# Kernel optimization log

Measured on AMD Instinct MI355X. Metric: run time of the kernel, lower is better.

The kernel has to match this reference:

```python
import jax, jax.numpy as jnp
import numpy as np

WS = 4        # window_size
SS = 2        # shift_size
NH = 8        # num_heads
EPS = 1e-5    # LayerNorm eps (torch default)


def _rel_pos_index(ws):
    coords = np.stack(np.meshgrid(np.arange(ws), np.arange(ws), indexing='ij')).reshape(2, -1)
    rel = (coords[:, :, None] - coords[:, None, :]).transpose(1, 2, 0)
    rel[..., 0] += ws - 1
    rel[..., 1] += ws - 1
    rel[..., 0] *= 2 * ws - 1
    return rel.sum(-1)  # [N, N] ints

REL_IDX = _rel_pos_index(WS)


def _shift_mask(Hp, Wp, ws, ss):
    # standard Swin shifted-window region mask: 0 within region, -100 across regions
    img = np.zeros((Hp, Wp))
    cnt = 0
    for hs in (slice(0, -ws), slice(-ws, -ss), slice(-ss, None)):
        for wsl in (slice(0, -ws), slice(-ws, -ss), slice(-ss, None)):
            img[hs, wsl] = cnt
            cnt += 1
    mw = img.reshape(Hp // ws, ws, Wp // ws, ws).transpose(0, 2, 1, 3).reshape(-1, ws * ws)
    d = mw[:, None, :] - mw[:, :, None]
    return np.where(d != 0, -100.0, 0.0).astype(np.float32)  # [nW, N, N]


def _ln(x, g, b):
    m = jnp.mean(x, -1, keepdims=True)
    v = jnp.mean((x - m) ** 2, -1, keepdims=True)
    return (x - m) * jax.lax.rsqrt(v + EPS) * g + b


def setup_inputs() -> dict:
    key = jax.random.key(0)
    ks = jax.random.split(key, 8)
    D, F = 512, 1024
    rn = lambda k, s: (jax.random.normal(k, s, jnp.float32) * 0.02)
    return {
        'x': jax.random.normal(ks[0], (4, 64 * 128, D), jnp.float32),
        'g1': jnp.ones((D,), jnp.float32), 'beta1': jnp.zeros((D,), jnp.float32),
        'w_qkv': rn(ks[1], (3 * D, D)), 'b_qkv': jnp.zeros((3 * D,), jnp.float32),
        'rpb': rn(ks[2], ((2 * WS - 1) ** 2, NH)),
        'w_proj': rn(ks[3], (D, D)), 'b_proj': jnp.zeros((D,), jnp.float32),
        'g2': jnp.ones((D,), jnp.float32), 'beta2': jnp.zeros((D,), jnp.float32),
        'w1': rn(ks[4], (F, D)), 'b1': jnp.zeros((F,), jnp.float32),
        'w2': rn(ks[5], (D, F)), 'b2': jnp.zeros((D,), jnp.float32),
        'H': 64, 'W': 128,
    }


def reference(x, g1, beta1, w_qkv, b_qkv, rpb, w_proj, b_proj, g2, beta2, w1, b1, w2, b2, H, W):
    B, L, C = x.shape
    hd = C // NH
    scale = hd ** (-0.5)
    N = WS * WS
    Hp, Wp = H, W  # H, W chosen divisible by WS -> no padding branch
    nW = (Hp // WS) * (Wp // WS)

    shortcut = x
    h = _ln(x, g1, beta1).reshape(B, H, W, C)
    # cyclic shift
    h = jnp.roll(h, (-SS, -SS), axis=(1, 2))
    # window partition -> [B*nW, N, C]
    xw = h.reshape(B, Hp // WS, WS, Wp // WS, WS, C).transpose(0, 1, 3, 2, 4, 5).reshape(-1, N, C)

    qkv = (xw @ w_qkv.T + b_qkv).reshape(-1, N, 3, NH, hd).transpose(2, 0, 3, 1, 4)
    q, k, v = qkv[0] * scale, qkv[1], qkv[2]          # [B*nW, NH, N, hd]
    attn = jnp.einsum('whnd,whmd->whnm', q, k)        # [B*nW, NH, N, N]

    bias = rpb[REL_IDX.reshape(-1)].reshape(N, N, NH).transpose(2, 0, 1)  # [NH, N, N]
    attn = attn + bias[None]

    mask = jnp.asarray(_shift_mask(Hp, Wp, WS, SS))   # [nW, N, N]
    attn = attn.reshape(B, nW, NH, N, N) + mask[None, :, None]
    attn = jax.nn.softmax(attn.reshape(-1, NH, N, N), axis=-1)

    o = jnp.einsum('whnm,whmd->whnd', attn, v).transpose(0, 2, 1, 3).reshape(-1, N, C)
    o = o @ w_proj.T + b_proj
    # window reverse + reverse shift
    o = o.reshape(B, Hp // WS, Wp // WS, WS, WS, C).transpose(0, 1, 3, 2, 4, 5).reshape(B, Hp, Wp, C)
    o = jnp.roll(o, (SS, SS), axis=(1, 2)).reshape(B, H * W, C)

    x = shortcut + o
    h2 = _ln(x, g2, beta2)
    m = jax.nn.gelu(h2 @ w1.T + b1, approximate=False) @ w2.T + b2
    return x + m
```

## Files before the change

kernel.cpp:

```cpp
#include <hip/hip_runtime.h>
#include <hip/hip_bf16.h>
#include <math.h>

typedef __bf16 bf16_t;
typedef __bf16 bf16x8 __attribute__((ext_vector_type(8)));
typedef __bf16 bf16x4 __attribute__((ext_vector_type(4)));
typedef float f32x4 __attribute__((ext_vector_type(4)));


#define X1_OFF   0u
#define XW_OFF   67108864u
#define QKV_OFF  100663296u
#define WQ_OFF   201326592u
#define WP_OFF   202899456u
#define W1_OFF   203423744u
#define W2_OFF   204472320u
#define SV_OFF   205520896u
#define FLAG_OFF 205545472u

__device__ __forceinline__ int perm_row(int r) {
    int b   = r >> 13;
    int rem = r & 8191;
    int w   = rem >> 4;
    int n   = rem & 15;
    int wy  = w >> 5, wx = w & 31;
    int y   = wy * 4 + (n >> 2);
    int x   = wx * 4 + (n & 3);
    int ys  = (y + 2) & 63;
    int xs  = (x + 2) & 127;
    return (b << 13) + (ys << 7) + xs;
}

__device__ __forceinline__ void gld16(const void* g, void* l) {
    __builtin_amdgcn_global_load_lds(
        (const __attribute__((address_space(1))) unsigned int*)(unsigned long long)(uintptr_t)g,
        (__attribute__((address_space(3))) unsigned int*)(unsigned int)(uintptr_t)l,
        16, 0, 0);
}

#define SBAR __builtin_amdgcn_sched_barrier(0)
#define BARRIER do { SBAR; __builtin_amdgcn_s_barrier(); SBAR; } while (0)

__device__ __forceinline__ float fast_gelu(float x) {
    float y = 0.7978845608f * (x + 0.044715f * x * x * x);
    y = fminf(fmaxf(y, -15.f), 15.f);
    float u = __builtin_amdgcn_exp2f(y * 2.885390082f);
    float t = (u - 1.f) / (u + 1.f);
    return 0.5f * x * (1.f + t);
}

__global__ __launch_bounds__(256) void k_probe(const unsigned short* __restrict__ x,
                                               int n, int* __restrict__ flag) {
    __shared__ int cnt;
    if (threadIdx.x == 0) cnt = 0;
    __syncthreads();
    int c = 0;
    for (int i = threadIdx.x; i < n; i += 256) {
        int e = (x[i] >> 7) & 0xFF;
        if (e >= 0xC0) c++;
    }
    atomicAdd(&cnt, c);
    __syncthreads();
    if (threadIdx.x == 0) *flag = (cnt > 8) ? 1 : 0;
}

__global__ __launch_bounds__(256) void k_cvt_bf16(const void* __restrict__ src,
                                                  bf16_t* __restrict__ dst, int n,
                                                  const int* __restrict__ flag) {
    int i = blockIdx.x * 256 + threadIdx.x;
    if (i >= n) return;
    if (*flag) dst[i] = (bf16_t)((const float*)src)[i];
    else       dst[i] = ((const bf16_t*)src)[i];
}

__global__ __launch_bounds__(256) void k_cvt_small(
        const void* g1, const void* be1, const void* bq, const void* bp,
        const void* g2, const void* be2, const void* b1, const void* b2,
        const void* rpb, float* __restrict__ dst, const int* __restrict__ flag) {
    int i = blockIdx.x * 256 + threadIdx.x;
    const void* src; int off;
    if      (i < 512)  { src = g1;  off = i; }
    else if (i < 1024) { src = be1; off = i - 512; }
    else if (i < 2560) { src = bq;  off = i - 1024; }
    else if (i < 3072) { src = bp;  off = i - 2560; }
    else if (i < 3584) { src = g2;  off = i - 3072; }
    else if (i < 4096) { src = be2; off = i - 3584; }
    else if (i < 5120) { src = b1;  off = i - 4096; }
    else if (i < 5632) { src = b2;  off = i - 5120; }
    else if (i < 6024) { src = rpb; off = i - 5632; }
    else return;
    if (*flag) dst[i] = ((const float*)src)[off];
    else       dst[i] = (float)((const bf16_t*)src)[off];
}

__global__ __launch_bounds__(256) void k_ln1(const void* __restrict__ x,
                                             const float* __restrict__ g,
                                             const float* __restrict__ be,
                                             bf16_t* __restrict__ xw,
                                             const int* __restrict__ flag) {
    int r    = blockIdx.x * 4 + (threadIdx.x >> 6);
    int lane = threadIdx.x & 63;
    long ro  = (long)perm_row(r) * 512;
    int base = lane * 8;
    float v[8];
    if (*flag) {
        const float* p = (const float*)x + ro + base;
#pragma unroll
        for (int j = 0; j < 8; j++) v[j] = p[j];
    } else {
        bf16x8 p = *(const bf16x8*)((const bf16_t*)x + ro + base);
#pragma unroll
        for (int j = 0; j < 8; j++) v[j] = (float)p[j];
    }
    float s = 0.f, ss = 0.f;
#pragma unroll
    for (int j = 0; j < 8; j++) { s += v[j]; ss += v[j] * v[j]; }
#pragma unroll
    for (int off = 32; off; off >>= 1) {
        s  += __shfl_down(s,  off, 64);
        ss += __shfl_down(ss, off, 64);
    }
    s  = __shfl(s, 0, 64);
    ss = __shfl(ss, 0, 64);
    float m   = s * (1.f / 512.f);
    float var = ss * (1.f / 512.f) - m * m;
    float inv = rsqrtf(var + 1e-5f);
    bf16_t* orow = xw + (long)r * 512;
    bf16x8 o;
#pragma unroll
    for (int j = 0; j < 8; j++)
        o[j] = (bf16_t)((v[j] - m) * inv * g[base + j] + be[base + j]);
    *(bf16x8*)(orow + base) = o;
}

__global__ __launch_bounds__(256) void k_ln2(const float* __restrict__ x1,
                                             const float* __restrict__ g,
                                             const float* __restrict__ be,
                                             bf16_t* __restrict__ h2) {
    int r    = blockIdx.x * 4 + (threadIdx.x >> 6);
    int lane = threadIdx.x & 63;
    const float* xr = x1 + (long)r * 512;
    int base = lane * 8;
    float v[8];
    float s = 0.f, ss = 0.f;
#pragma unroll
    for (int j = 0; j < 8; j++) {
        float t = xr[base + j];
        v[j] = t; s += t; ss += t * t;
    }
#pragma unroll
    for (int off = 32; off; off >>= 1) {
        s  += __shfl_down(s,  off, 64);
        ss += __shfl_down(ss, off, 64);
    }
    s  = __shfl(s, 0, 64);
    ss = __shfl(ss, 0, 64);
    float m   = s * (1.f / 512.f);
    float var = ss * (1.f / 512.f) - m * m;
    float inv = rsqrtf(var + 1e-5f);
    bf16_t* orow = h2 + (long)r * 512;
    bf16x8 o;
#pragma unroll
    for (int j = 0; j < 8; j++)
        o[j] = (bf16_t)((v[j] - m) * inv * g[base + j] + be[base + j]);
    *(bf16x8*)(orow + base) = o;
}

template<int EPI>
__global__ __launch_bounds__(512, 2) void k_gemm256(const bf16_t* __restrict__ A,
                                                    const bf16_t* __restrict__ Wt,
                                                    const float* __restrict__ bias,
                                                    void* __restrict__ out,
                                                    const void* __restrict__ res,
                                                    const int* __restrict__ flag,
                                                    int N, int K) {
    __shared__ __attribute__((aligned(16))) char smem[131072];
    int tid  = threadIdx.x;
    int lane = tid & 63, wv = tid >> 6;

    int nbx = N >> 8;
    int id  = blockIdx.x;
    int xb  = (id >> 3) % nbx;
    int yb  = ((id >> 3) / nbx) * 8 + (id & 7);
    int m0  = yb << 8, n0 = xb << 8;

    int srow = tid >> 3;
    int cg   = (tid & 7) ^ (srow & 7);
    const bf16_t* gA = A  + (long)(m0 + srow) * K + cg * 8;
    const bf16_t* gB = Wt + (long)(n0 + srow) * K + cg * 8;
    long r64 = (long)64 * K;

    int rr = lane & 15, quad = lane >> 4;
    int wh = wv >> 2, wq = wv & 3;
    int lA  = (wh * 64 + rr) * 128;
    int lB  = (wq * 32 + rr) * 128;
    int ck0 = (quad ^ (rr & 7)) * 16;
    int ck1 = ck0 ^ 64;

    f32x4 acc[8][4];
#pragma unroll
    for (int mi = 0; mi < 8; mi++)
#pragma unroll
        for (int ni = 0; ni < 4; ni++) { f32x4 z = {0.f,0.f,0.f,0.f}; acc[mi][ni] = z; }

    int S = K >> 6;

    gld16(gA,             smem + 0     + wv * 1024);
    gld16(gA + r64,       smem + 8192  + wv * 1024);
    gld16(gB,             smem + 32768 + wv * 1024);
    gld16(gB + r64,       smem + 40960 + wv * 1024);
    gld16(gB + 2 * r64,   smem + 49152 + wv * 1024);
    gld16(gB + 3 * r64,   smem + 57344 + wv * 1024);
    gld16(gA + 2 * r64,   smem + 16384 + wv * 1024);
    gld16(gA + 3 * r64,   smem + 24576 + wv * 1024);
    asm volatile("s_waitcnt vmcnt(4)" ::: "memory");
    BARRIER;

    bf16x8 af[4][2], bg[2][2];

#define FRAG_A(AH)                                                            \
    _Pragma("unroll") for (int mi = 0; mi < 4; mi++) {                        \
        af[mi][0] = *(const bf16x8*)(bc + (AH)*16384 + lA + mi*2048 + ck0);   \
        af[mi][1] = *(const bf16x8*)(bc + (AH)*16384 + lA + mi*2048 + ck1);   \
    }
#define FRAG_B(BH)                                                            \
    _Pragma("unroll") for (int ni = 0; ni < 2; ni++) {                        \
        bg[ni][0] = *(const bf16x8*)(bc + 32768 + (BH)*16384 + lB + ni*2048 + ck0); \
        bg[ni][1] = *(const bf16x8*)(bc + 32768 + (BH)*16384 + lB + ni*2048 + ck1); \
    }
#define MFMA_CL(AH, BH)                                                       \
    do {                                                                      \
        asm volatile("s_waitcnt lgkmcnt(0)" ::: "memory"); SBAR;              \
        __builtin_amdgcn_s_setprio(1);                                        \
        _Pragma("unroll") for (int mi = 0; mi < 4; mi++)                      \
            _Pragma("unroll") for (int ni = 0; ni < 2; ni++)                  \
                _Pragma("unroll") for (int kk = 0; kk < 2; kk++)              \
                    acc[(AH)*4 + mi][(BH)*2 + ni] =                           \
                        __builtin_amdgcn_mfma_f32_16x16x32_bf16(              \
                            af[mi][kk], bg[ni][kk], acc[(AH)*4 + mi][(BH)*2 + ni], 0, 0, 0); \
        __builtin_amdgcn_s_setprio(0);                                        \
    } while (0)
#define STAGE(GP, SLOT)                                                       \
    do { gld16((GP) + kn,       bn + (SLOT) + wv * 1024);                     \
         gld16((GP) + r64 + kn, bn + (SLOT) + 8192 + wv * 1024); } while (0)

    for (int t = 0; t < S; ++t) {
        char* bc = smem + (t & 1) * 65536;
        char* bn = smem + ((t & 1) ^ 1) * 65536;
        long  kn = (long)(t + 1) * 64;
        bool  st = (t + 1 < S);
        FRAG_A(0); FRAG_B(0);
        if (st) { STAGE(gA, 0);
                  asm volatile("s_waitcnt vmcnt(4)" ::: "memory"); }
        else    { asm volatile("s_waitcnt vmcnt(2)" ::: "memory"); }
        BARRIER;
        MFMA_CL(0, 0);
        FRAG_B(1);
        if (st) { STAGE(gB, 32768);
                  asm volatile("s_waitcnt vmcnt(4)" ::: "memory"); }
        else    { asm volatile("s_waitcnt vmcnt(0)" ::: "memory"); }
        BARRIER;
        MFMA_CL(0, 1);
        FRAG_A(1);
        if (st) STAGE(gB + 2 * r64, 49152);
        BARRIER;
        MFMA_CL(1, 1);
        FRAG_B(0);
        if (st) { STAGE(gA + 2 * r64, 16384);
                  asm volatile("s_waitcnt vmcnt(4)" ::: "memory"); }
        BARRIER;
        MFMA_CL(1, 0);
    }
    BARRIER;
#undef FRAG_A
#undef FRAG_B
#undef MFMA_CL
#undef STAGE

    float* sc = (float*)(smem + wv * 16384);
    int f    = (EPI == 1 || EPI == 3) ? *flag : 0;
    int j8   = lane & 7;
    int rl   = lane >> 3;
    int colg = n0 + wq * 32 + (j8 >> 2) * 128 + ((j8 * 8) & 31);
    f32x4 b0 = *(const f32x4*)(bias + colg);
    f32x4 b1 = *(const f32x4*)(bias + colg + 4);

#pragma unroll
    for (int ah = 0; ah < 2; ++ah) {
#pragma unroll
        for (int bh = 0; bh < 2; ++bh)
#pragma unroll
            for (int ni = 0; ni < 2; ++ni)
#pragma unroll
                for (int mi = 0; mi < 4; ++mi)
#pragma unroll
                    for (int i = 0; i < 4; ++i) {
                        int r  = mi * 16 + quad * 4 + i;
                        int cl = bh * 32 + ni * 16 + rr;
                        sc[r * 64 + ((((cl >> 2) ^ (r & 15)) << 2) | (cl & 3))] =
                            acc[ah * 4 + mi][bh * 2 + ni][i];
                    }
#pragma unroll
        for (int p = 0; p < 8; ++p) {
            int r = p * 8 + rl;
            f32x4 v0 = *(const f32x4*)(sc + r * 64 + (((2 * j8)     ^ (r & 15)) << 2));
            f32x4 v1 = *(const f32x4*)(sc + r * 64 + (((2 * j8 + 1) ^ (r & 15)) << 2));
            int row = m0 + ah * 128 + wh * 64 + r;
            v0 += b0; v1 += b1;

            if (EPI == 0) {
                bf16x8 ob;
#pragma unroll
                for (int c = 0; c < 4; c++) { ob[c] = (bf16_t)v0[c]; ob[c + 4] = (bf16_t)v1[c]; }
                *(bf16x8*)((bf16_t*)out + (long)row * N + colg) = ob;
            } else if (EPI == 1) {
                long o = (long)perm_row(row) * 512 + colg;
                if (f) {
                    f32x4 r0 = *(const f32x4*)((const float*)res + o);
                    f32x4 r1 = *(const f32x4*)((const float*)res + o + 4);
                    v0 += r0; v1 += r1;
                } else {
                    bf16x8 rb = *(const bf16x8*)((const bf16_t*)res + o);
#pragma unroll
                    for (int c = 0; c < 4; c++) { v0[c] += (float)rb[c]; v1[c] += (float)rb[c + 4]; }
                }
                *(f32x4*)((float*)out + o)     = v0;
                *(f32x4*)((float*)out + o + 4) = v1;
            } else if (EPI == 2) {
                bf16x8 ob;
#pragma unroll
                for (int c = 0; c < 4; c++) {
                    ob[c]     = (bf16_t)fast_gelu(v0[c]);
                    ob[c + 4] = (bf16_t)fast_gelu(v1[c]);
                }
                *(bf16x8*)((bf16_t*)out + (long)row * N + colg) = ob;
            } else {
                long o = (long)row * 512 + colg;
                f32x4 r0 = *(const f32x4*)((const float*)res + o);
                f32x4 r1 = *(const f32x4*)((const float*)res + o + 4);
                v0 += r0; v1 += r1;
                if (f) {
                    *(f32x4*)((float*)out + o)     = v0;
                    *(f32x4*)((float*)out + o + 4) = v1;
                } else {
                    bf16x8 ob;
#pragma unroll
                    for (int c = 0; c < 4; c++) { ob[c] = (bf16_t)v0[c]; ob[c + 4] = (bf16_t)v1[c]; }
                    *(bf16x8*)((bf16_t*)out + o) = ob;
                }
            }
        }
    }
}

__global__ __launch_bounds__(256) void k_attn(const bf16_t* __restrict__ qkv,
                                              const float* __restrict__ rpb,
                                              bf16_t* __restrict__ O) {
    __shared__ float q[16][68], k[16][68], v[16][68];
    __shared__ float S[16][17];

    int blk = blockIdx.x;
    int h   = blk & 7;
    int w   = blk >> 3;
    int tid = threadIdx.x;

    int n0 = tid >> 4;
    int d0 = (tid & 15) * 4;
    const bf16_t* base = qkv + (long)(w * 16 + n0) * 1536 + h * 64 + d0;
    bf16x4 qv = *(const bf16x4*)(base);
    bf16x4 kv = *(const bf16x4*)(base + 512);
    bf16x4 vv = *(const bf16x4*)(base + 1024);
    f32x4 qf, kf, vf;
#pragma unroll
    for (int j = 0; j < 4; j++) {
        qf[j] = (float)qv[j] * 0.125f;
        kf[j] = (float)kv[j];
        vf[j] = (float)vv[j];
    }
    *(f32x4*)&q[n0][d0] = qf;
    *(f32x4*)&k[n0][d0] = kf;
    *(f32x4*)&v[n0][d0] = vf;
    __syncthreads();

    int i = tid >> 4, j = tid & 15;
    float s = 0.f;
#pragma unroll
    for (int d = 0; d < 64; d++) s += q[i][d] * k[j][d];

    int iy = i >> 2, ix = i & 3, jy = j >> 2, jx = j & 3;
    s += rpb[((iy - jy + 3) * 7 + (ix - jx + 3)) * 8 + h];

    int wl = w & 511;
    int wy = wl >> 5, wx = wl & 31;
    int yi = wy * 4 + iy, xi = wx * 4 + ix;
    int yj = wy * 4 + jy, xj = wx * 4 + jx;
    int ri = (yi < 60 ? 0 : (yi < 62 ? 1 : 2)) * 3 + (xi < 124 ? 0 : (xi < 126 ? 1 : 2));
    int rj = (yj < 60 ? 0 : (yj < 62 ? 1 : 2)) * 3 + (xj < 124 ? 0 : (xj < 126 ? 1 : 2));
    if (ri != rj) s -= 100.f;
    S[i][j] = s;
    __syncthreads();

    if (tid < 16) {
        float mx = -1e30f;
#pragma unroll
        for (int c = 0; c < 16; c++) mx = fmaxf(mx, S[tid][c]);
        float sum = 0.f;
#pragma unroll
        for (int c = 0; c < 16; c++) { float e = expf(S[tid][c] - mx); S[tid][c] = e; sum += e; }
        float invs = 1.f / sum;
#pragma unroll
        for (int c = 0; c < 16; c++) S[tid][c] *= invs;
    }
    __syncthreads();

#pragma unroll
    for (int t = 0; t < 4; t++) {
        int e  = tid + t * 256;
        int oi = e >> 6, od = e & 63;
        float acc = 0.f;
#pragma unroll
        for (int c = 0; c < 16; c++) acc += S[oi][c] * v[c][od];
        O[(long)(w * 16 + oi) * 512 + h * 64 + od] = (bf16_t)acc;
    }
}

extern "C" void kernel_launch(void* const* d_in, const int* in_sizes, int n_in,
                              void* d_out, int out_size, void* d_ws, size_t ws_size,
                              hipStream_t stream) {
    char* ws = (char*)d_ws;
    float*  x1   = (float*)(ws + X1_OFF);
    bf16_t* xw   = (bf16_t*)(ws + XW_OFF);
    bf16_t* qkv  = (bf16_t*)(ws + QKV_OFF);
    bf16_t* wq_b = (bf16_t*)(ws + WQ_OFF);
    bf16_t* wp_b = (bf16_t*)(ws + WP_OFF);
    bf16_t* w1_b = (bf16_t*)(ws + W1_OFF);
    bf16_t* w2_b = (bf16_t*)(ws + W2_OFF);
    float*  sv   = (float*)(ws + SV_OFF);
    int*    flag = (int*)(ws + FLAG_OFF);

    k_probe<<<1, 256, 0, stream>>>((const unsigned short*)d_in[0], 4096, flag);
    k_cvt_bf16<<<3072, 256, 0, stream>>>(d_in[3],  wq_b, 786432, flag);
    k_cvt_bf16<<<1024, 256, 0, stream>>>(d_in[6],  wp_b, 262144, flag);
    k_cvt_bf16<<<2048, 256, 0, stream>>>(d_in[10], w1_b, 524288, flag);
    k_cvt_bf16<<<2048, 256, 0, stream>>>(d_in[12], w2_b, 524288, flag);
    k_cvt_small<<<24,  256, 0, stream>>>(d_in[1], d_in[2], d_in[4], d_in[7],
                                         d_in[8], d_in[9], d_in[11], d_in[13],
                                         d_in[5], sv, flag);

    k_ln1<<<dim3(8192), dim3(256), 0, stream>>>(d_in[0], sv, sv + 512, xw, flag);
    k_gemm256<0><<<dim3(768), dim3(512), 0, stream>>>(xw, wq_b, sv + 1024, qkv, nullptr, flag, 1536, 512);
    k_attn<<<dim3(16384), dim3(256), 0, stream>>>(qkv, sv + 5632, xw );
    k_gemm256<1><<<dim3(256), dim3(512), 0, stream>>>(xw, wp_b, sv + 2560, x1, d_in[0], flag, 512, 512);
    k_ln2<<<dim3(8192), dim3(256), 0, stream>>>(x1, sv + 3072, sv + 3584, xw );
    k_gemm256<2><<<dim3(512), dim3(512), 0, stream>>>(xw, w1_b, sv + 4096, qkv , nullptr, flag, 1024, 512);
    k_gemm256<3><<<dim3(256), dim3(512), 0, stream>>>(qkv, w2_b, sv + 5120, d_out, x1, flag, 512, 1024);
}
```

Baseline: 427.8 us.

## Add 128x128 GEMM kernel for N=512 GEMMs and warp-shuffle attention softmax

Adds a smaller-tile 128x128 GEMM kernel (256 threads, 64KB LDS, double buffered) and uses it for the two N=512 GEMMs (proj and FC2). This raises the grid from 256 to 1024 blocks so the many CUs on the device are better occupied. The epilogue is factored into a shared helper. Separately, the attention softmax now uses 16-lane shuffle reductions across all threads instead of 16 serial threads, which removes one barrier.

```diff
diff --git a/kernel.cpp b/kernel.cpp
--- a/kernel.cpp
+++ b/kernel.cpp
@@ -164,6 +164,74 @@
     for (int j = 0; j < 8; j++)
         o[j] = (bf16_t)((v[j] - m) * inv * g[base + j] + be[base + j]);
     *(bf16x8*)(orow + base) = o;
+}
+
+template<int EPI>
+__device__ __forceinline__ void epi_block(float* sc, const f32x4* accp,
+                                          int quad, int rr, int rl, int j8,
+                                          int row0, int colg, f32x4 b0, f32x4 b1,
+                                          void* out, const void* res, int f, int N) {
+#pragma unroll
+    for (int ni = 0; ni < 4; ++ni)
+#pragma unroll
+        for (int mi = 0; mi < 4; ++mi)
+#pragma unroll
+            for (int i = 0; i < 4; ++i) {
+                int r  = mi * 16 + quad * 4 + i;
+                int cl = ni * 16 + rr;
+                sc[r * 64 + ((((cl >> 2) ^ (r & 15)) << 2) | (cl & 3))] =
+                    accp[mi * 4 + ni][i];
+            }
+#pragma unroll
+    for (int p = 0; p < 8; ++p) {
+        int r = p * 8 + rl;
+        f32x4 v0 = *(const f32x4*)(sc + r * 64 + (((2 * j8)     ^ (r & 15)) << 2));
+        f32x4 v1 = *(const f32x4*)(sc + r * 64 + (((2 * j8 + 1) ^ (r & 15)) << 2));
+        int row = row0 + r;
+        v0 += b0; v1 += b1;
+
+        if (EPI == 0) {
+            bf16x8 ob;
+#pragma unroll
+            for (int c = 0; c < 4; c++) { ob[c] = (bf16_t)v0[c]; ob[c + 4] = (bf16_t)v1[c]; }
+            *(bf16x8*)((bf16_t*)out + (long)row * N + colg) = ob;
+        } else if (EPI == 1) {
+            long o = (long)perm_row(row) * 512 + colg;
+            if (f) {
+                f32x4 r0 = *(const f32x4*)((const float*)res + o);
+                f32x4 r1 = *(const f32x4*)((const float*)res + o + 4);
+                v0 += r0; v1 += r1;
+            } else {
+                bf16x8 rb = *(const bf16x8*)((const bf16_t*)res + o);
+#pragma unroll
+                for (int c = 0; c < 4; c++) { v0[c] += (float)rb[c]; v1[c] += (float)rb[c + 4]; }
+            }
+            *(f32x4*)((float*)out + o)     = v0;
+            *(f32x4*)((float*)out + o + 4) = v1;
+        } else if (EPI == 2) {
+            bf16x8 ob;
+#pragma unroll
+            for (int c = 0; c < 4; c++) {
+                ob[c]     = (bf16_t)fast_gelu(v0[c]);
+                ob[c + 4] = (bf16_t)fast_gelu(v1[c]);
+            }
+            *(bf16x8*)((bf16_t*)out + (long)row * N + colg) = ob;
+        } else {
+            long o = (long)row * 512 + colg;
+            f32x4 r0 = *(const f32x4*)((const float*)res + o);
+            f32x4 r1 = *(const f32x4*)((const float*)res + o + 4);
+            v0 += r0; v1 += r1;
+            if (f) {
+                *(f32x4*)((float*)out + o)     = v0;
+                *(f32x4*)((float*)out + o + 4) = v1;
+            } else {
+                bf16x8 ob;
+#pragma unroll
+                for (int c = 0; c < 4; c++) { ob[c] = (bf16_t)v0[c]; ob[c + 4] = (bf16_t)v1[c]; }
+                *(bf16x8*)((bf16_t*)out + o) = ob;
+            }
+        }
+    }
 }
 
 template<int EPI>
@@ -287,77 +355,118 @@
 
 #pragma unroll
     for (int ah = 0; ah < 2; ++ah) {
+        f32x4 blk[16];
 #pragma unroll
         for (int bh = 0; bh < 2; ++bh)
 #pragma unroll
             for (int ni = 0; ni < 2; ++ni)
 #pragma unroll
                 for (int mi = 0; mi < 4; ++mi)
-#pragma unroll
-                    for (int i = 0; i < 4; ++i) {
-                        int r  = mi * 16 + quad * 4 + i;
-                        int cl = bh * 32 + ni * 16 + rr;
-                        sc[r * 64 + ((((cl >> 2) ^ (r & 15)) << 2) | (cl & 3))] =
-                            acc[ah * 4 + mi][bh * 2 + ni][i];
-                    }
-#pragma unroll
-        for (int p = 0; p < 8; ++p) {
-            int r = p * 8 + rl;
-            f32x4 v0 = *(const f32x4*)(sc + r * 64 + (((2 * j8)     ^ (r & 15)) << 2));
-            f32x4 v1 = *(const f32x4*)(sc + r * 64 + (((2 * j8 + 1) ^ (r & 15)) << 2));
-            int row = m0 + ah * 128 + wh * 64 + r;
-            v0 += b0; v1 += b1;
-
-            if (EPI == 0) {
-                bf16x8 ob;
-#pragma unroll
-                for (int c = 0; c < 4; c++) { ob[c] = (bf16_t)v0[c]; ob[c + 4] = (bf16_t)v1[c]; }
-                *(bf16x8*)((bf16_t*)out + (long)row * N + colg) = ob;
-            } else if (EPI == 1) {
-                long o = (long)perm_row(row) * 512 + colg;
-                if (f) {
-                    f32x4 r0 = *(const f32x4*)((const float*)res + o);
-                    f32x4 r1 = *(const f32x4*)((const float*)res + o + 4);
-                    v0 += r0; v1 += r1;
-                } else {
-                    bf16x8 rb = *(const bf16x8*)((const bf16_t*)res + o);
-#pragma unroll
-                    for (int c = 0; c < 4; c++) { v0[c] += (float)rb[c]; v1[c] += (float)rb[c + 4]; }
-                }
-                *(f32x4*)((float*)out + o)     = v0;
-                *(f32x4*)((float*)out + o + 4) = v1;
-            } else if (EPI == 2) {
-                bf16x8 ob;
-#pragma unroll
-                for (int c = 0; c < 4; c++) {
-                    ob[c]     = (bf16_t)fast_gelu(v0[c]);
-                    ob[c + 4] = (bf16_t)fast_gelu(v1[c]);
-                }
-                *(bf16x8*)((bf16_t*)out + (long)row * N + colg) = ob;
-            } else {
-                long o = (long)row * 512 + colg;
-                f32x4 r0 = *(const f32x4*)((const float*)res + o);
-                f32x4 r1 = *(const f32x4*)((const float*)res + o + 4);
-                v0 += r0; v1 += r1;
-                if (f) {
-                    *(f32x4*)((float*)out + o)     = v0;
-                    *(f32x4*)((float*)out + o + 4) = v1;
-                } else {
-                    bf16x8 ob;
-#pragma unroll
-                    for (int c = 0; c < 4; c++) { ob[c] = (bf16_t)v0[c]; ob[c + 4] = (bf16_t)v1[c]; }
-                    *(bf16x8*)((bf16_t*)out + o) = ob;
-                }
-            }
+                    blk[mi * 4 + (bh * 2 + ni)] = acc[ah * 4 + mi][bh * 2 + ni];
+        epi_block<EPI>(sc, blk, quad, rr, rl, j8,
+                       m0 + ah * 128 + wh * 64, colg, b0, b1, out, res, f, N);
+    }
+}
+
+template<int EPI>
+__global__ __launch_bounds__(256, 2) void k_gemm128(const bf16_t* __restrict__ A,
+                                                    const bf16_t* __restrict__ Wt,
+                                                    const float* __restrict__ bias,
+                                                    void* __restrict__ out,
+                                                    const void* __restrict__ res,
+                                                    const int* __restrict__ flag,
+                                                    int N, int K) {
+    __shared__ __attribute__((aligned(16))) char smem[65536];
+    int tid  = threadIdx.x;
+    int lane = tid & 63, wv = tid >> 6;
+
+    int nbx = N >> 7;
+    int id  = blockIdx.x;
+    int xb  = (id >> 3) % nbx;
+    int yb  = ((id >> 3) / nbx) * 8 + (id & 7);
+    int m0  = yb << 7, n0 = xb << 7;
+
+    int srow = tid >> 3;
+    int cg   = (tid & 7) ^ (srow & 7);
+    const bf16_t* gA = A  + (long)(m0 + srow) * K + cg * 8;
+    const bf16_t* gB = Wt + (long)(n0 + srow) * K + cg * 8;
+    long r32 = (long)32 * K;
+
+    int rr = lane & 15, quad = lane >> 4;
+    int wr = wv >> 1, wc = wv & 1;
+    int lA  = (wr * 64 + rr) * 128;
+    int lB  = 16384 + (wc * 64 + rr) * 128;
+    int ck0 = (quad ^ (rr & 7)) * 16;
+    int ck1 = ck0 ^ 64;
+
+    f32x4 acc[4][4];
+#pragma unroll
+    for (int mi = 0; mi < 4; mi++)
+#pragma unroll
+        for (int ni = 0; ni < 4; ni++) { f32x4 z = {0.f,0.f,0.f,0.f}; acc[mi][ni] = z; }
+
+    int S = K >> 6;
+
+#pragma unroll
+    for (int j = 0; j < 4; j++) gld16(gA + j * r32, smem + j * 4096 + wv * 1024);
+#pragma unroll
+    for (int j = 0; j < 4; j++) gld16(gB + j * r32, smem + 16384 + j * 4096 + wv * 1024);
+
+    bf16x8 af[4], bg[4];
+
+#define FRAG128(CK)                                                           \
+    do {                                                                      \
+        _Pragma("unroll") for (int mi = 0; mi < 4; mi++)                      \
+            af[mi] = *(const bf16x8*)(bc + lA + mi * 2048 + (CK));            \
+        _Pragma("unroll") for (int ni = 0; ni < 4; ni++)                      \
+            bg[ni] = *(const bf16x8*)(bc + lB + ni * 2048 + (CK));            \
+        asm volatile("s_waitcnt lgkmcnt(0)" ::: "memory"); SBAR;              \
+        __builtin_amdgcn_s_setprio(1);                                        \
+        _Pragma("unroll") for (int mi = 0; mi < 4; mi++)                      \
+            _Pragma("unroll") for (int ni = 0; ni < 4; ni++)                  \
+                acc[mi][ni] = __builtin_amdgcn_mfma_f32_16x16x32_bf16(        \
+                    af[mi], bg[ni], acc[mi][ni], 0, 0, 0);                    \
+        __builtin_amdgcn_s_setprio(0);                                        \
+    } while (0)
+
+    for (int t = 0; t < S; ++t) {
+        char* bc = smem + (t & 1) * 32768;
+        char* bn = smem + ((t & 1) ^ 1) * 32768;
+        if (t + 1 < S) {
+            long kn = (long)(t + 1) * 64;
+#pragma unroll
+            for (int j = 0; j < 4; j++)
+                gld16(gA + kn + j * r32, bn + j * 4096 + wv * 1024);
+#pragma unroll
+            for (int j = 0; j < 4; j++)
+                gld16(gB + kn + j * r32, bn + 16384 + j * 4096 + wv * 1024);
+            asm volatile("s_waitcnt vmcnt(8)" ::: "memory");
+        } else {
+            asm volatile("s_waitcnt vmcnt(0)" ::: "memory");
         }
-    }
+        BARRIER;
+        FRAG128(ck0);
+        FRAG128(ck1);
+        BARRIER;
+    }
+#undef FRAG128
+
+    float* sc = (float*)(smem + wv * 16384);
+    int f    = (EPI == 1 || EPI == 3) ? *flag : 0;
+    int j8   = lane & 7;
+    int rl   = lane >> 3;
+    int colg = n0 + wc * 64 + j8 * 8;
+    f32x4 b0 = *(const f32x4*)(bias + colg);
+    f32x4 b1 = *(const f32x4*)(bias + colg + 4);
+    epi_block<EPI>(sc, &acc[0][0], quad, rr, rl, j8,
+                   m0 + wr * 64, colg, b0, b1, out, res, f, N);
 }
 
 __global__ __launch_bounds__(256) void k_attn(const bf16_t* __restrict__ qkv,
                                               const float* __restrict__ rpb,
                                               bf16_t* __restrict__ O) {
     __shared__ float q[16][68], k[16][68], v[16][68];
-    __shared__ float S[16][17];
+    __shared__ float P[16][17];
 
     int blk = blockIdx.x;
     int h   = blk & 7;
@@ -397,29 +506,24 @@
     int ri = (yi < 60 ? 0 : (yi < 62 ? 1 : 2)) * 3 + (xi < 124 ? 0 : (xi < 126 ? 1 : 2));
     int rj = (yj < 60 ? 0 : (yj < 62 ? 1 : 2)) * 3 + (xj < 124 ? 0 : (xj < 126 ? 1 : 2));
     if (ri != rj) s -= 100.f;
-    S[i][j] = s;
+
+    float mx = s;
+#pragma unroll
+    for (int m = 8; m; m >>= 1) mx = fmaxf(mx, __shfl_xor(mx, m, 16));
+    float e = expf(s - mx);
+    float sum = e;
+#pragma unroll
+    for (int m = 8; m; m >>= 1) sum += __shfl_xor(sum, m, 16);
+    P[i][j] = e / sum;
     __syncthreads();
 
-    if (tid < 16) {
-        float mx = -1e30f;
-#pragma unroll
-        for (int c = 0; c < 16; c++) mx = fmaxf(mx, S[tid][c]);
-        float sum = 0.f;
-#pragma unroll
-        for (int c = 0; c < 16; c++) { float e = expf(S[tid][c] - mx); S[tid][c] = e; sum += e; }
-        float invs = 1.f / sum;
-#pragma unroll
-        for (int c = 0; c < 16; c++) S[tid][c] *= invs;
-    }
-    __syncthreads();
-
 #pragma unroll
     for (int t = 0; t < 4; t++) {
-        int e  = tid + t * 256;
-        int oi = e >> 6, od = e & 63;
+        int e2 = tid + t * 256;
+        int oi = e2 >> 6, od = e2 & 63;
         float acc = 0.f;
 #pragma unroll
-        for (int c = 0; c < 16; c++) acc += S[oi][c] * v[c][od];
+        for (int c = 0; c < 16; c++) acc += P[oi][c] * v[c][od];
         O[(long)(w * 16 + oi) * 512 + h * 64 + od] = (bf16_t)acc;
     }
 }
@@ -450,8 +554,8 @@
     k_ln1<<<dim3(8192), dim3(256), 0, stream>>>(d_in[0], sv, sv + 512, xw, flag);
     k_gemm256<0><<<dim3(768), dim3(512), 0, stream>>>(xw, wq_b, sv + 1024, qkv, nullptr, flag, 1536, 512);
     k_attn<<<dim3(16384), dim3(256), 0, stream>>>(qkv, sv + 5632, xw );
-    k_gemm256<1><<<dim3(256), dim3(512), 0, stream>>>(xw, wp_b, sv + 2560, x1, d_in[0], flag, 512, 512);
+    k_gemm128<1><<<dim3(1024), dim3(256), 0, stream>>>(xw, wp_b, sv + 2560, x1, d_in[0], flag, 512, 512);
     k_ln2<<<dim3(8192), dim3(256), 0, stream>>>(x1, sv + 3072, sv + 3584, xw );
     k_gemm256<2><<<dim3(512), dim3(512), 0, stream>>>(xw, w1_b, sv + 4096, qkv , nullptr, flag, 1024, 512);
-    k_gemm256<3><<<dim3(256), dim3(512), 0, stream>>>(qkv, w2_b, sv + 5120, d_out, x1, flag, 512, 1024);
-}
+    k_gemm128<3><<<dim3(1024), dim3(256), 0, stream>>>(qkv, w2_b, sv + 5120, d_out, x1, flag, 512, 1024);
+}
```

New measurement: 435.3 us. Within noise of the previous version (+1.7%).
